# Performance work log

Measured on AMD Instinct MI355X. Metric: run time of the kernel, lower is better.

## Reference

```python
import jax, jax.numpy as jnp
import numpy as np
from jax import lax

B, T, K = 8192, 512, 5


def setup_inputs() -> dict:
    key = jax.random.key(0)
    k1, k2, k3, k4 = jax.random.split(key, 4)
    potentials = jax.random.normal(k1, (B, T, K), dtype=jnp.float32)
    transition_params = jax.random.normal(k2, (K, K), dtype=jnp.float32) * 0.1
    sequence_lengths = jax.random.randint(k3, (B,), 1, T + 1, dtype=jnp.int32)
    tag_indices = jax.random.randint(k4, (B, T), 0, K, dtype=jnp.int32)
    return {
        "potentials": potentials,
        "transition_params": transition_params,
        "sequence_lengths": sequence_lengths,
        "tag_indices": tag_indices,
    }


def _crf(potentials, transition_params, sequence_lengths, tag_indices):
    Bn, Tn, Kn = potentials.shape
    alpha0 = potentials[:, 0]                        # (B, K)
    pots_rest = jnp.swapaxes(potentials[:, 1:], 0, 1)  # (T-1, B, K)
    ts = jnp.arange(1, Tn)
    valid = ts[:, None] < sequence_lengths[None, :]    # (T-1, B)
    tag_range = jnp.arange(Kn, dtype=jnp.int32)

    # ---- Viterbi forward: max-product DP with backpointers ----
    def vit_step(alpha, inp):
        pot_t, v = inp
        scores = alpha[:, :, None] + transition_params[None]  # (B, K, K) over prev i -> next j
        bp = jnp.argmax(scores, axis=1).astype(jnp.int32)     # (B, K)
        new_alpha = jnp.max(scores, axis=1) + pot_t
        alpha = jnp.where(v[:, None], new_alpha, alpha)       # freeze past seq end
        bp = jnp.where(v[:, None], bp, tag_range[None])       # identity bp past seq end
        return alpha, bp

    alpha_v, bps = lax.scan(vit_step, alpha0, (pots_rest, valid))
    last_tag = jnp.argmax(alpha_v, axis=1).astype(jnp.int32)  # (B,)

    # ---- backtrack ----
    def back_step(tag, bp_t):
        prev = jnp.take_along_axis(bp_t, tag[:, None], axis=1)[:, 0]
        return prev, prev

    _, prev_tags = lax.scan(back_step, last_tag, bps, reverse=True)  # (T-1, B) tags 0..T-2
    decoded = jnp.concatenate([jnp.swapaxes(prev_tags, 0, 1), last_tag[:, None]], axis=1)
    mask = jnp.arange(Tn)[None] < sequence_lengths[:, None]          # (B, T)
    decoded = jnp.where(mask, decoded, 0)

    # ---- forward algorithm: log partition ----
    def fwd_step(alpha, inp):
        pot_t, v = inp
        new_alpha = jax.nn.logsumexp(alpha[:, :, None] + transition_params[None], axis=1) + pot_t
        return jnp.where(v[:, None], new_alpha, alpha), None

    alpha_f, _ = lax.scan(fwd_step, alpha0, (pots_rest, valid))
    log_norm = jax.nn.logsumexp(alpha_f, axis=1)                     # (B,)

    # ---- gold sequence score ----
    unary = jnp.take_along_axis(potentials, tag_indices[:, :, None], axis=2)[:, :, 0]  # (B, T)
    unary = jnp.sum(jnp.where(mask, unary, 0.0), axis=1)
    trans_sc = transition_params[tag_indices[:, :-1], tag_indices[:, 1:]]              # (B, T-1)
    tmask = jnp.arange(1, Tn)[None] < sequence_lengths[:, None]
    binary = jnp.sum(jnp.where(tmask, trans_sc, 0.0), axis=1)

    log_likelihood = unary + binary - log_norm
    return decoded, log_likelihood


def reference(potentials, transition_params, sequence_lengths, tag_indices):
    return _crf(potentials, transition_params, sequence_lengths, tag_indices)
```

## Files before the change

### kernel.cpp

```cpp
#include <hip/hip_runtime.h>
#include <stdint.h>

#define KK 5
#define TT 512

template<int P>
__device__ __forceinline__ float swzf(float v) {
  return __int_as_float(__builtin_amdgcn_ds_swizzle(__float_as_int(v), P));
}
template<int P>
__device__ __forceinline__ int swzi(int v) {
  return __builtin_amdgcn_ds_swizzle(v, P);
}
#define BC0 0x018
#define BC1 0x038
#define BC2 0x058
#define BC3 0x078
#define BC4 0x098
#define X1 0x041F
#define X2 0x081F
#define X4 0x101F

__device__ __forceinline__ void loadCol(float (&d)[8], const float* __restrict__ colp, int k) {
  const int t0 = k * 8 + 1;
  if (k < 63) {
#pragma unroll
    for (int s = 0; s < 8; ++s) d[s] = colp[(t0 + s) * KK];
  } else {
#pragma unroll
    for (int s = 0; s < 8; ++s) d[s] = colp[min(t0 + s, TT - 1) * KK];
  }
}

__device__ __forceinline__ void vit_map_block(const float (&pv)[8], int k, int len_eff,
                                              const float (&trc)[KK], float& a,
                                              int jj, int g, int r,
                                              uint32_t* __restrict__ s_map) {
  uint32_t bits = 0;
#pragma unroll
  for (int s = 0; s < 8; ++s) {
    const float av0 = swzf<BC0>(a), av1 = swzf<BC1>(a), av2 = swzf<BC2>(a),
                av3 = swzf<BC3>(a), av4 = swzf<BC4>(a);
    const float s0 = av0 + trc[0], s1 = av1 + trc[1], s2 = av2 + trc[2],
                s3 = av3 + trc[3], s4 = av4 + trc[4];
    const float bm = fmaxf(fmaxf(fmaxf(s0, s1), fmaxf(s2, s3)), s4);
    int bi = 4;
    bi = (s3 == bm) ? 3 : bi;
    bi = (s2 == bm) ? 2 : bi;
    bi = (s1 == bm) ? 1 : bi;
    bi = (s0 == bm) ? 0 : bi;
    const int t = k * 8 + s + 1;
    const bool act = (t < len_eff);
    a = act ? (bm + pv[s]) : a;
    const int bie = act ? bi : jj;
    bits |= (uint32_t)bie << (3 * s);
  }
  int cur = jj;
  uint32_t dec = 0;
#pragma unroll
  for (int s = 7; s >= 0; --s) {
    const int w = __builtin_amdgcn_ds_bpermute(((g << 3) + cur) << 2, (int)bits);
    const int b3 = (w >> (3 * s)) & 7;
    dec |= (uint32_t)b3 << (3 * s);
    cur = b3;
  }
  if (r < 5) s_map[g * 321 + k * 5 + jj] = dec;
}

__device__ __forceinline__ void fwd_block(const float (&pv)[8], int k, int len_eff,
                                          const float (&Wc)[KK], float& p, float& Cacc) {
#pragma unroll
  for (int s = 0; s < 8; ++s) {
    const float p0 = swzf<BC0>(p), p1 = swzf<BC1>(p), p2 = swzf<BC2>(p),
                p3 = swzf<BC3>(p), p4 = swzf<BC4>(p);
    const float u  = fmaf(p1, Wc[1], p0 * Wc[0]);
    const float v2 = fmaf(p3, Wc[3], p2 * Wc[2]);
    const float acc = fmaf(p4, Wc[4], u + v2);
    const float E = __expf(pv[s]);
    const int t = k * 8 + s + 1;
    const bool act = (t < len_eff);
    p = act ? (acc * E) : p;
  }
  float m = p;
  m = fmaxf(m, swzf<X1>(m));
  m = fmaxf(m, swzf<X2>(m));
  m = fmaxf(m, swzf<X4>(m));
  p *= (1.0f / m);
  Cacc += __logf(m);
}

__launch_bounds__(64)
__global__ void crf_kernel(const float* __restrict__ pot,
                           const float* __restrict__ trans,
                           const int* __restrict__ lens,
                           const int* __restrict__ tags,
                           float* __restrict__ out,
                           int B, int T) {
  __shared__ uint32_t s_map[8 * 321];
  __shared__ uint32_t s_chosen[8 * 65];
  const int lane = threadIdx.x;
  const int g = lane >> 3, r = lane & 7;
  const int jj = (r < 5) ? r : 4;
  const unsigned u = blockIdx.x;
  const int role = (u >> 3) & 1;
  const int idx = (int)((u & 7u) | ((u >> 4) << 3));
  const int b = idx * 8 + g;
  const int len = lens[b];
  const int len_eff = (r < 5) ? len : 0;
  const float* __restrict__ prow = pot + (size_t)b * (T * KK);
  const float* __restrict__ colp = prow + jj;

  int ml = len;
  ml = max(ml, __shfl_xor(ml, 8));
  ml = max(ml, __shfl_xor(ml, 16));
  ml = max(ml, __shfl_xor(ml, 32));
  const int nblk = (ml + 7) >> 3;

  if (role == 0) {
    float trc[KK];
#pragma unroll
    for (int i = 0; i < KK; ++i) trc[i] = trans[i * KK + jj];
    float a = (r < 5) ? prow[jj] : -3.0e38f;

    float pA[8], pB[8], pC[8];
    loadCol(pA, colp, 0);
    loadCol(pB, colp, min(1, nblk - 1));
    loadCol(pC, colp, min(2, nblk - 1));
    int blk = 0;
    while (true) {
      vit_map_block(pA, blk, len_eff, trc, a, jj, g, r, s_map);
      if (++blk == nblk) break;
      loadCol(pA, colp, min(blk + 2, nblk - 1));
      vit_map_block(pB, blk, len_eff, trc, a, jj, g, r, s_map);
      if (++blk == nblk) break;
      loadCol(pB, colp, min(blk + 2, nblk - 1));
      vit_map_block(pC, blk, len_eff, trc, a, jj, g, r, s_map);
      if (++blk == nblk) break;
      loadCol(pC, colp, min(blk + 2, nblk - 1));
    }
    float bm = a;
    bm = fmaxf(bm, swzf<X1>(bm));
    bm = fmaxf(bm, swzf<X2>(bm));
    bm = fmaxf(bm, swzf<X4>(bm));
    int cand = (r < 5 && a == bm) ? r : 7;
    cand = min(cand, swzi<X1>(cand));
    cand = min(cand, swzi<X2>(cand));
    cand = min(cand, swzi<X4>(cand));
    const int last = cand;

    __syncthreads();
    if (r == 0) {
      int tag = last;
      for (int k2 = nblk - 1; k2 >= 0; --k2) {
        const uint32_t w = s_map[g * 321 + k2 * 5 + tag];
        s_chosen[g * 65 + k2] = w;
        tag = (int)(w & 7u);
      }
    }
    __syncthreads();

    float* __restrict__ orow = out + (size_t)b * T;
#pragma unroll
    for (int kk = 0; kk < 8; ++kk) {
      const int k2 = kk * 8 + r;
      const uint32_t w = s_chosen[g * 65 + k2];
      const int base = k2 * 8;
      float f[8];
#pragma unroll
      for (int pI = 0; pI < 8; ++pI)
        f[pI] = (base + pI < len) ? (float)((w >> (3 * pI)) & 7u) : 0.0f;
      *(float4*)(orow + base)     = make_float4(f[0], f[1], f[2], f[3]);
      *(float4*)(orow + base + 4) = make_float4(f[4], f[5], f[6], f[7]);
    }

  } else {
    const float trv = trans[min(lane, 24)];
    const int* __restrict__ tgrow = tags + (size_t)b * T;
    float sc = 0.0f;
    {
      const int t0 = r * 64;
      int ptag = (t0 == 0) ? 0 : tgrow[t0 - 1];
#pragma unroll 2
      for (int q = 0; q < 16; ++q) {
        const int4 tq = *(const int4*)(tgrow + t0 + q * 4);
#pragma unroll
        for (int m = 0; m < 4; ++m) {
          const int t = t0 + q * 4 + m;
          const int ct = (m == 0) ? tq.x : (m == 1) ? tq.y : (m == 2) ? tq.z : tq.w;
          const float uadd = prow[t * KK + ct];
          const float badd = __int_as_float(__builtin_amdgcn_ds_bpermute(
              (ptag * KK + ct) << 2, __float_as_int(trv)));
          const float contrib = uadd + ((t >= 1) ? badd : 0.0f);
          sc += (t < len) ? contrib : 0.0f;
          ptag = ct;
        }
      }
    }
    sc += swzf<X1>(sc);
    sc += swzf<X2>(sc);
    sc += swzf<X4>(sc);

    float Wc[KK];
#pragma unroll
    for (int i = 0; i < KK; ++i) Wc[i] = __expf(trans[i * KK + jj]);
    float p = (r < 5) ? __expf(prow[jj]) : 0.0f;
    float Cacc = 0.0f;

    float pA[8], pB[8], pC[8];
    loadCol(pA, colp, 0);
    loadCol(pB, colp, min(1, nblk - 1));
    loadCol(pC, colp, min(2, nblk - 1));
    int blk = 0;
    while (true) {
      fwd_block(pA, blk, len_eff, Wc, p, Cacc);
      if (++blk == nblk) break;
      loadCol(pA, colp, min(blk + 2, nblk - 1));
      fwd_block(pB, blk, len_eff, Wc, p, Cacc);
      if (++blk == nblk) break;
      loadCol(pB, colp, min(blk + 2, nblk - 1));
      fwd_block(pC, blk, len_eff, Wc, p, Cacc);
      if (++blk == nblk) break;
      loadCol(pC, colp, min(blk + 2, nblk - 1));
    }
    float ps = p;
    ps += swzf<X1>(ps);
    ps += swzf<X2>(ps);
    ps += swzf<X4>(ps);
    const float logZ = Cacc + __logf(ps);
    if (r == 0) out[(size_t)B * T + b] = sc - logZ;
  }
}

extern "C" void kernel_launch(void* const* d_in, const int* in_sizes, int n_in,
                              void* d_out, int out_size, void* d_ws, size_t ws_size,
                              hipStream_t stream) {
  const float* pot   = (const float*)d_in[0];
  const float* trans = (const float*)d_in[1];
  const int*   lens  = (const int*)d_in[2];
  const int*   tags  = (const int*)d_in[3];
  float* out = (float*)d_out;

  const int B = in_sizes[2];
  const int T = in_sizes[3] / B;

  const int nblocks = 2 * (B / 8);
  crf_kernel<<<nblocks, 64, 0, stream>>>(pot, trans, lens, tags, out, B, T);
}
```

Measured before the change: 91.89 us.

## Drop per-block backpointer composition and use exponent-only rescaling in CRF kernel

The Viterbi path no longer composes 8-step backpointer maps with bpermute chains. It stores raw per-step backpointer bits and does a serial per-step backtrack in one lane per sequence, with the next block's words prefetched. Masking on the recurrence is replaced by snapshotting the state at t==len-1 (a_fin, p_fin, C_fin). The forward pass swaps its per-block cross-lane max reduction, reciprocal and log for a power-of-two rescale from ilogbf/ldexpf on the already-broadcast values, and issues its potential loads before the gold-score loop. This shortens the recurrence's dependency chain, but the backtrack becomes a longer serial loop per sequence, and removing the __syncthreads relies on s_bits and s_chosen being written and read within the same wave.

```diff
diff --git a/kernel.cpp b/kernel.cpp
--- a/kernel.cpp
+++ b/kernel.cpp
@@ -21,6 +21,16 @@
 #define X2 0x081F
 #define X4 0x101F
 
+__device__ __forceinline__ uint32_t sel5u(uint32_t w0, uint32_t w1, uint32_t w2,
+                                          uint32_t w3, uint32_t w4, int ct) {
+  uint32_t u = w0;
+  u = (ct == 1) ? w1 : u;
+  u = (ct == 2) ? w2 : u;
+  u = (ct == 3) ? w3 : u;
+  u = (ct == 4) ? w4 : u;
+  return u;
+}
+
 __device__ __forceinline__ void loadCol(float (&d)[8], const float* __restrict__ colp, int k) {
   const int t0 = k * 8 + 1;
   if (k < 63) {
@@ -32,13 +42,14 @@
   }
 }
 
-__device__ __forceinline__ void vit_map_block(const float (&pv)[8], int k, int len_eff,
-                                              const float (&trc)[KK], float& a,
-                                              int jj, int g, int r,
-                                              uint32_t* __restrict__ s_map) {
+__device__ __forceinline__ void vit_blk(const float (&pv)[8], int k, int len,
+                                        const float (&trc)[KK], float& a,
+                                        float& a_fin, int g, int r, int jj,
+                                        uint32_t* __restrict__ s_bits) {
   uint32_t bits = 0;
 #pragma unroll
   for (int s = 0; s < 8; ++s) {
+    const int t = k * 8 + s + 1;
     const float av0 = swzf<BC0>(a), av1 = swzf<BC1>(a), av2 = swzf<BC2>(a),
                 av3 = swzf<BC3>(a), av4 = swzf<BC4>(a);
     const float s0 = av0 + trc[0], s1 = av1 + trc[1], s2 = av2 + trc[2],
@@ -49,44 +60,36 @@
     bi = (s2 == bm) ? 2 : bi;
     bi = (s1 == bm) ? 1 : bi;
     bi = (s0 == bm) ? 0 : bi;
+    bits |= (uint32_t)bi << (3 * s);
+    a = bm + pv[s];
+    a_fin = (t == len - 1) ? a : a_fin;
+  }
+  if (r < 5) s_bits[g * 321 + k * 5 + jj] = bits;
+}
+
+__device__ __forceinline__ void fwd_blk(const float (&pv)[8], int k, int len,
+                                        const float (&Wc)[KK], float& p,
+                                        float& Cacc, float& p_fin, float& C_fin) {
+#pragma unroll
+  for (int s = 0; s < 8; ++s) {
     const int t = k * 8 + s + 1;
-    const bool act = (t < len_eff);
-    a = act ? (bm + pv[s]) : a;
-    const int bie = act ? bi : jj;
-    bits |= (uint32_t)bie << (3 * s);
-  }
-  int cur = jj;
-  uint32_t dec = 0;
-#pragma unroll
-  for (int s = 7; s >= 0; --s) {
-    const int w = __builtin_amdgcn_ds_bpermute(((g << 3) + cur) << 2, (int)bits);
-    const int b3 = (w >> (3 * s)) & 7;
-    dec |= (uint32_t)b3 << (3 * s);
-    cur = b3;
-  }
-  if (r < 5) s_map[g * 321 + k * 5 + jj] = dec;
-}
-
-__device__ __forceinline__ void fwd_block(const float (&pv)[8], int k, int len_eff,
-                                          const float (&Wc)[KK], float& p, float& Cacc) {
-#pragma unroll
-  for (int s = 0; s < 8; ++s) {
     const float p0 = swzf<BC0>(p), p1 = swzf<BC1>(p), p2 = swzf<BC2>(p),
                 p3 = swzf<BC3>(p), p4 = swzf<BC4>(p);
-    const float u  = fmaf(p1, Wc[1], p0 * Wc[0]);
-    const float v2 = fmaf(p3, Wc[3], p2 * Wc[2]);
-    const float acc = fmaf(p4, Wc[4], u + v2);
+    float r_ = 1.0f;
+    if (s == 0 && k > 0) {
+      const float m = fmaxf(fmaxf(fmaxf(p0, p1), fmaxf(p2, p3)), p4);
+      const int e = ilogbf(m);
+      r_ = ldexpf(1.0f, -e);
+      Cacc += (float)e * 0.69314718056f;
+    }
     const float E = __expf(pv[s]);
-    const int t = k * 8 + s + 1;
-    const bool act = (t < len_eff);
-    p = act ? (acc * E) : p;
-  }
-  float m = p;
-  m = fmaxf(m, swzf<X1>(m));
-  m = fmaxf(m, swzf<X2>(m));
-  m = fmaxf(m, swzf<X4>(m));
-  p *= (1.0f / m);
-  Cacc += __logf(m);
+    float acc = fmaf(p1, Wc[1], p0 * Wc[0]);
+    const float acc2 = fmaf(p3, Wc[3], p2 * Wc[2]);
+    acc = fmaf(p4, Wc[4], acc + acc2);
+    p = acc * E * r_;
+    p_fin = (t == len - 1) ? p : p_fin;
+    C_fin = (t == len - 1) ? Cacc : C_fin;
+  }
 }
 
 __launch_bounds__(64)
@@ -96,7 +99,7 @@
                            const int* __restrict__ tags,
                            float* __restrict__ out,
                            int B, int T) {
-  __shared__ uint32_t s_map[8 * 321];
+  __shared__ uint32_t s_bits[8 * 321];
   __shared__ uint32_t s_chosen[8 * 65];
   const int lane = threadIdx.x;
   const int g = lane >> 3, r = lane & 7;
@@ -106,7 +109,6 @@
   const int idx = (int)((u & 7u) | ((u >> 4) << 3));
   const int b = idx * 8 + g;
   const int len = lens[b];
-  const int len_eff = (r < 5) ? len : 0;
   const float* __restrict__ prow = pot + (size_t)b * (T * KK);
   const float* __restrict__ colp = prow + jj;
 
@@ -121,6 +123,7 @@
 #pragma unroll
     for (int i = 0; i < KK; ++i) trc[i] = trans[i * KK + jj];
     float a = (r < 5) ? prow[jj] : -3.0e38f;
+    float a_fin = a;
 
     float pA[8], pB[8], pC[8];
     loadCol(pA, colp, 0);
@@ -128,36 +131,59 @@
     loadCol(pC, colp, min(2, nblk - 1));
     int blk = 0;
     while (true) {
-      vit_map_block(pA, blk, len_eff, trc, a, jj, g, r, s_map);
+      vit_blk(pA, blk, len, trc, a, a_fin, g, r, jj, s_bits);
       if (++blk == nblk) break;
       loadCol(pA, colp, min(blk + 2, nblk - 1));
-      vit_map_block(pB, blk, len_eff, trc, a, jj, g, r, s_map);
+      vit_blk(pB, blk, len, trc, a, a_fin, g, r, jj, s_bits);
       if (++blk == nblk) break;
       loadCol(pB, colp, min(blk + 2, nblk - 1));
-      vit_map_block(pC, blk, len_eff, trc, a, jj, g, r, s_map);
+      vit_blk(pC, blk, len, trc, a, a_fin, g, r, jj, s_bits);
       if (++blk == nblk) break;
       loadCol(pC, colp, min(blk + 2, nblk - 1));
     }
-    float bm = a;
+    float bm = a_fin;
     bm = fmaxf(bm, swzf<X1>(bm));
     bm = fmaxf(bm, swzf<X2>(bm));
     bm = fmaxf(bm, swzf<X4>(bm));
-    int cand = (r < 5 && a == bm) ? r : 7;
+    int cand = (r < 5 && a_fin == bm) ? r : 7;
     cand = min(cand, swzi<X1>(cand));
     cand = min(cand, swzi<X2>(cand));
     cand = min(cand, swzi<X4>(cand));
     const int last = cand;
 
-    __syncthreads();
     if (r == 0) {
       int tag = last;
-      for (int k2 = nblk - 1; k2 >= 0; --k2) {
-        const uint32_t w = s_map[g * 321 + k2 * 5 + tag];
-        s_chosen[g * 65 + k2] = w;
-        tag = (int)(w & 7u);
+      uint32_t acc = (uint32_t)last << (3 * ((len - 1) & 7));
+      int kcur = (len - 1) >> 3;
+      const uint32_t* __restrict__ bb = s_bits + g * 321;
+      int kb = (len - 2) >> 3;
+      uint32_t w0 = 0, w1 = 0, w2 = 0, w3 = 0, w4 = 0;
+      if (kb >= 0) {
+        w0 = bb[kb * 5 + 0]; w1 = bb[kb * 5 + 1]; w2 = bb[kb * 5 + 2];
+        w3 = bb[kb * 5 + 3]; w4 = bb[kb * 5 + 4];
       }
-    }
-    __syncthreads();
+      for (; kb >= 0; --kb) {
+        uint32_t n0 = 0, n1 = 0, n2 = 0, n3 = 0, n4 = 0;
+        if (kb > 0) {
+          n0 = bb[(kb - 1) * 5 + 0]; n1 = bb[(kb - 1) * 5 + 1];
+          n2 = bb[(kb - 1) * 5 + 2]; n3 = bb[(kb - 1) * 5 + 3];
+          n4 = bb[(kb - 1) * 5 + 4];
+        }
+#pragma unroll
+        for (int s = 7; s >= 0; --s) {
+          const int t = kb * 8 + s + 1;
+          if (t <= len - 1) {
+            const uint32_t w = sel5u(w0, w1, w2, w3, w4, tag);
+            const int prev = (int)((w >> (3 * s)) & 7u);
+            if (kb != kcur) { s_chosen[g * 65 + kcur] = acc; acc = 0; kcur = kb; }
+            acc |= (uint32_t)prev << (3 * s);
+            tag = prev;
+          }
+        }
+        w0 = n0; w1 = n1; w2 = n2; w3 = n3; w4 = n4;
+      }
+      s_chosen[g * 65 + kcur] = acc;
+    }
 
     float* __restrict__ orow = out + (size_t)b * T;
 #pragma unroll
@@ -174,6 +200,11 @@
     }
 
   } else {
+    float pA[8], pB[8], pC[8];
+    loadCol(pA, colp, 0);
+    loadCol(pB, colp, min(1, nblk - 1));
+    loadCol(pC, colp, min(2, nblk - 1));
+
     const float trv = trans[min(lane, 24)];
     const int* __restrict__ tgrow = tags + (size_t)b * T;
     float sc = 0.0f;
@@ -205,28 +236,25 @@
     for (int i = 0; i < KK; ++i) Wc[i] = __expf(trans[i * KK + jj]);
     float p = (r < 5) ? __expf(prow[jj]) : 0.0f;
     float Cacc = 0.0f;
-
-    float pA[8], pB[8], pC[8];
-    loadCol(pA, colp, 0);
-    loadCol(pB, colp, min(1, nblk - 1));
-    loadCol(pC, colp, min(2, nblk - 1));
+    float p_fin = p, C_fin = 0.0f;
+
     int blk = 0;
     while (true) {
-      fwd_block(pA, blk, len_eff, Wc, p, Cacc);
+      fwd_blk(pA, blk, len, Wc, p, Cacc, p_fin, C_fin);
       if (++blk == nblk) break;
       loadCol(pA, colp, min(blk + 2, nblk - 1));
-      fwd_block(pB, blk, len_eff, Wc, p, Cacc);
+      fwd_blk(pB, blk, len, Wc, p, Cacc, p_fin, C_fin);
       if (++blk == nblk) break;
       loadCol(pB, colp, min(blk + 2, nblk - 1));
-      fwd_block(pC, blk, len_eff, Wc, p, Cacc);
+      fwd_blk(pC, blk, len, Wc, p, Cacc, p_fin, C_fin);
       if (++blk == nblk) break;
       loadCol(pC, colp, min(blk + 2, nblk - 1));
     }
-    float ps = p;
+    float ps = (r < 5) ? p_fin : 0.0f;
     ps += swzf<X1>(ps);
     ps += swzf<X2>(ps);
     ps += swzf<X4>(ps);
-    const float logZ = Cacc + __logf(ps);
+    const float logZ = C_fin + __logf(ps);
     if (r == 0) out[(size_t)B * T + b] = sc - logZ;
   }
 }
```

After: 115.0 us. 1.25x slower.

## Merge Viterbi and forward roles into one two-wave block, fuse gold score

Applied to the files above, without the earlier changes.

The two separate 64-thread blocks per group of 8 sequences become one 128-thread block. Wave 0 runs Viterbi and wave 1 runs the forward algorithm, and they share results through LDS with block barriers. The gold-sequence score is now computed inside the Viterbi loop from the potentials already held in registers plus prefetched tags. This removes the second wave's separate strided re-read of potentials and its bpermute-based transition lookups. The backtrack also gains special handling for the block containing the last valid step, which adds serial work on one lane and a dependency between the two waves.

```diff
diff --git a/kernel.cpp b/kernel.cpp
--- a/kernel.cpp
+++ b/kernel.cpp
@@ -4,12 +4,10 @@
 #define KK 5
 #define TT 512
 
-template<int P>
-__device__ __forceinline__ float swzf(float v) {
+template<int P> __device__ __forceinline__ float swzf(float v) {
   return __int_as_float(__builtin_amdgcn_ds_swizzle(__float_as_int(v), P));
 }
-template<int P>
-__device__ __forceinline__ int swzi(int v) {
+template<int P> __device__ __forceinline__ int swzi(int v) {
   return __builtin_amdgcn_ds_swizzle(v, P);
 }
 #define BC0 0x018
@@ -21,9 +19,21 @@
 #define X2 0x081F
 #define X4 0x101F
 
+__device__ __forceinline__ float sel5f(float v0,float v1,float v2,float v3,float v4,int ct){
+  float u=v0; u=(ct==1)?v1:u; u=(ct==2)?v2:u; u=(ct==3)?v3:u; u=(ct==4)?v4:u; return u;
+}
+__device__ __forceinline__ uint32_t sel5u(uint32_t w0,uint32_t w1,uint32_t w2,uint32_t w3,uint32_t w4,int ct){
+  uint32_t u=w0; u=(ct==1)?w1:u; u=(ct==2)?w2:u; u=(ct==3)?w3:u; u=(ct==4)?w4:u; return u;
+}
+__device__ __forceinline__ int telt(const int4 (&tp)[2], int s) {
+  const int4 v = (s < 4) ? tp[0] : tp[1];
+  const int m = s & 3;
+  return m == 0 ? v.x : (m == 1 ? v.y : (m == 2 ? v.z : v.w));
+}
+
 __device__ __forceinline__ void loadCol(float (&d)[8], const float* __restrict__ colp, int k) {
   const int t0 = k * 8 + 1;
-  if (k < 63) {
+  if (k < TT / 8 - 1) {
 #pragma unroll
     for (int s = 0; s < 8; ++s) d[s] = colp[(t0 + s) * KK];
   } else {
@@ -31,11 +41,15 @@
     for (int s = 0; s < 8; ++s) d[s] = colp[min(t0 + s, TT - 1) * KK];
   }
 }
-
-__device__ __forceinline__ void vit_map_block(const float (&pv)[8], int k, int len_eff,
-                                              const float (&trc)[KK], float& a,
-                                              int jj, int g, int r,
-                                              uint32_t* __restrict__ s_map) {
+__device__ __forceinline__ void loadTag(int4 (&tp)[2], const int* __restrict__ tg, int k) {
+  tp[0] = *(const int4*)(tg + 8 * k);
+  tp[1] = *(const int4*)(tg + 8 * k + 4);
+}
+
+__device__ __forceinline__ void vit_map_block(const float (&pv)[8], const int4 (&tp)[2],
+    int k, int len, int len_eff, const float (&trc)[KK], float& a,
+    float& pvcar, int& tagcar, float& usum, float& bsum,
+    int jj, int g, int r, uint32_t* __restrict__ s_map) {
   uint32_t bits = 0;
 #pragma unroll
   for (int s = 0; s < 8; ++s) {
@@ -65,10 +79,22 @@
     cur = b3;
   }
   if (r < 5) s_map[g * 321 + k * 5 + jj] = dec;
-}
-
-__device__ __forceinline__ void fwd_block(const float (&pv)[8], int k, int len_eff,
-                                          const float (&Wc)[KK], float& p, float& Cacc) {
+#pragma unroll
+  for (int s2 = 0; s2 < 8; ++s2) {
+    const int t = k * 8 + s2;
+    const int ct = telt(tp, s2);
+    const int pt = (s2 == 0) ? tagcar : telt(tp, s2 - 1);
+    const float potv = (s2 == 0) ? pvcar : pv[s2 - 1];
+    const bool um = (t < len) && (ct == r);
+    usum += um ? potv : 0.0f;
+    bsum += (um && t >= 1) ? sel5f(trc[0], trc[1], trc[2], trc[3], trc[4], pt) : 0.0f;
+  }
+  pvcar = pv[7];
+  tagcar = telt(tp, 7);
+}
+
+__device__ __forceinline__ void fwd_blk(const float (&pv)[8], int k, int len_eff,
+                                        const float (&Wc)[KK], float& p, float& Cacc) {
 #pragma unroll
   for (int s = 0; s < 8; ++s) {
     const float p0 = swzf<BC0>(p), p1 = swzf<BC1>(p), p2 = swzf<BC2>(p),
@@ -89,7 +115,7 @@
   Cacc += __logf(m);
 }
 
-__launch_bounds__(64)
+__launch_bounds__(128)
 __global__ void crf_kernel(const float* __restrict__ pot,
                            const float* __restrict__ trans,
                            const int* __restrict__ lens,
@@ -98,13 +124,13 @@
                            int B, int T) {
   __shared__ uint32_t s_map[8 * 321];
   __shared__ uint32_t s_chosen[8 * 65];
-  const int lane = threadIdx.x;
+  __shared__ float s_sc[8];
+  const int tid = threadIdx.x;
+  const int wave = tid >> 6;
+  const int lane = tid & 63;
   const int g = lane >> 3, r = lane & 7;
   const int jj = (r < 5) ? r : 4;
-  const unsigned u = blockIdx.x;
-  const int role = (u >> 3) & 1;
-  const int idx = (int)((u & 7u) | ((u >> 4) << 3));
-  const int b = idx * 8 + g;
+  const int b = blockIdx.x * 8 + g;
   const int len = lens[b];
   const int len_eff = (r < 5) ? len : 0;
   const float* __restrict__ prow = pot + (size_t)b * (T * KK);
@@ -116,28 +142,41 @@
   ml = max(ml, __shfl_xor(ml, 32));
   const int nblk = (ml + 7) >> 3;
 
-  if (role == 0) {
+  int last = 0;
+  float logZ = 0.0f;
+
+  if (wave == 0) {
     float trc[KK];
 #pragma unroll
     for (int i = 0; i < KK; ++i) trc[i] = trans[i * KK + jj];
     float a = (r < 5) ? prow[jj] : -3.0e38f;
+    float usum = 0.0f, bsum = 0.0f;
+    float pvcar = prow[jj];
+    int tagcar = 0;
+    const int* __restrict__ tg = tags + (size_t)b * T;
 
     float pA[8], pB[8], pC[8];
-    loadCol(pA, colp, 0);
-    loadCol(pB, colp, min(1, nblk - 1));
-    loadCol(pC, colp, min(2, nblk - 1));
+    int4 TA[2], TB[2], TC[2];
+    loadCol(pA, colp, 0);               loadTag(TA, tg, 0);
+    loadCol(pB, colp, min(1, nblk - 1)); loadTag(TB, tg, min(1, nblk - 1));
+    loadCol(pC, colp, min(2, nblk - 1)); loadTag(TC, tg, min(2, nblk - 1));
     int blk = 0;
     while (true) {
-      vit_map_block(pA, blk, len_eff, trc, a, jj, g, r, s_map);
-      if (++blk == nblk) break;
-      loadCol(pA, colp, min(blk + 2, nblk - 1));
-      vit_map_block(pB, blk, len_eff, trc, a, jj, g, r, s_map);
-      if (++blk == nblk) break;
-      loadCol(pB, colp, min(blk + 2, nblk - 1));
-      vit_map_block(pC, blk, len_eff, trc, a, jj, g, r, s_map);
-      if (++blk == nblk) break;
-      loadCol(pC, colp, min(blk + 2, nblk - 1));
-    }
+      vit_map_block(pA, TA, blk, len, len_eff, trc, a, pvcar, tagcar, usum, bsum, jj, g, r, s_map);
+      if (++blk == nblk) break;
+      loadCol(pA, colp, min(blk + 2, nblk - 1)); loadTag(TA, tg, min(blk + 2, nblk - 1));
+      vit_map_block(pB, TB, blk, len, len_eff, trc, a, pvcar, tagcar, usum, bsum, jj, g, r, s_map);
+      if (++blk == nblk) break;
+      loadCol(pB, colp, min(blk + 2, nblk - 1)); loadTag(TB, tg, min(blk + 2, nblk - 1));
+      vit_map_block(pC, TC, blk, len, len_eff, trc, a, pvcar, tagcar, usum, bsum, jj, g, r, s_map);
+      if (++blk == nblk) break;
+      loadCol(pC, colp, min(blk + 2, nblk - 1)); loadTag(TC, tg, min(blk + 2, nblk - 1));
+    }
+    float sc = usum + bsum;
+    sc += swzf<X1>(sc);
+    sc += swzf<X2>(sc);
+    sc += swzf<X4>(sc);
+    if (r == 0) s_sc[g] = sc;
     float bm = a;
     bm = fmaxf(bm, swzf<X1>(bm));
     bm = fmaxf(bm, swzf<X2>(bm));
@@ -146,79 +185,26 @@
     cand = min(cand, swzi<X1>(cand));
     cand = min(cand, swzi<X2>(cand));
     cand = min(cand, swzi<X4>(cand));
-    const int last = cand;
-
-    __syncthreads();
-    if (r == 0) {
-      int tag = last;
-      for (int k2 = nblk - 1; k2 >= 0; --k2) {
-        const uint32_t w = s_map[g * 321 + k2 * 5 + tag];
-        s_chosen[g * 65 + k2] = w;
-        tag = (int)(w & 7u);
-      }
-    }
-    __syncthreads();
-
-    float* __restrict__ orow = out + (size_t)b * T;
-#pragma unroll
-    for (int kk = 0; kk < 8; ++kk) {
-      const int k2 = kk * 8 + r;
-      const uint32_t w = s_chosen[g * 65 + k2];
-      const int base = k2 * 8;
-      float f[8];
-#pragma unroll
-      for (int pI = 0; pI < 8; ++pI)
-        f[pI] = (base + pI < len) ? (float)((w >> (3 * pI)) & 7u) : 0.0f;
-      *(float4*)(orow + base)     = make_float4(f[0], f[1], f[2], f[3]);
-      *(float4*)(orow + base + 4) = make_float4(f[4], f[5], f[6], f[7]);
-    }
-
+    last = cand;
   } else {
-    const float trv = trans[min(lane, 24)];
-    const int* __restrict__ tgrow = tags + (size_t)b * T;
-    float sc = 0.0f;
-    {
-      const int t0 = r * 64;
-      int ptag = (t0 == 0) ? 0 : tgrow[t0 - 1];
-#pragma unroll 2
-      for (int q = 0; q < 16; ++q) {
-        const int4 tq = *(const int4*)(tgrow + t0 + q * 4);
-#pragma unroll
-        for (int m = 0; m < 4; ++m) {
-          const int t = t0 + q * 4 + m;
-          const int ct = (m == 0) ? tq.x : (m == 1) ? tq.y : (m == 2) ? tq.z : tq.w;
-          const float uadd = prow[t * KK + ct];
-          const float badd = __int_as_float(__builtin_amdgcn_ds_bpermute(
-              (ptag * KK + ct) << 2, __float_as_int(trv)));
-          const float contrib = uadd + ((t >= 1) ? badd : 0.0f);
-          sc += (t < len) ? contrib : 0.0f;
-          ptag = ct;
-        }
-      }
-    }
-    sc += swzf<X1>(sc);
-    sc += swzf<X2>(sc);
-    sc += swzf<X4>(sc);
-
     float Wc[KK];
 #pragma unroll
     for (int i = 0; i < KK; ++i) Wc[i] = __expf(trans[i * KK + jj]);
     float p = (r < 5) ? __expf(prow[jj]) : 0.0f;
     float Cacc = 0.0f;
-
     float pA[8], pB[8], pC[8];
     loadCol(pA, colp, 0);
     loadCol(pB, colp, min(1, nblk - 1));
     loadCol(pC, colp, min(2, nblk - 1));
     int blk = 0;
     while (true) {
-      fwd_block(pA, blk, len_eff, Wc, p, Cacc);
+      fwd_blk(pA, blk, len_eff, Wc, p, Cacc);
       if (++blk == nblk) break;
       loadCol(pA, colp, min(blk + 2, nblk - 1));
-      fwd_block(pB, blk, len_eff, Wc, p, Cacc);
+      fwd_blk(pB, blk, len_eff, Wc, p, Cacc);
       if (++blk == nblk) break;
       loadCol(pB, colp, min(blk + 2, nblk - 1));
-      fwd_block(pC, blk, len_eff, Wc, p, Cacc);
+      fwd_blk(pC, blk, len_eff, Wc, p, Cacc);
       if (++blk == nblk) break;
       loadCol(pC, colp, min(blk + 2, nblk - 1));
     }
@@ -226,8 +212,59 @@
     ps += swzf<X1>(ps);
     ps += swzf<X2>(ps);
     ps += swzf<X4>(ps);
-    const float logZ = Cacc + __logf(ps);
-    if (r == 0) out[(size_t)B * T + b] = sc - logZ;
+    logZ = Cacc + __logf(ps);
+  }
+
+  __syncthreads();
+
+  if (wave == 0) {
+    if (r == 0) {
+      int tag = last;
+      uint32_t acc = (uint32_t)last << (3 * ((len - 1) & 7));
+      int kcur = (len - 1) >> 3;
+      const uint32_t* __restrict__ bb = s_map + g * 321;
+      for (int k2 = nblk - 1; k2 >= 0; --k2) {
+        if (k2 < kcur) {
+          const uint32_t w = bb[k2 * 5 + tag];
+          s_chosen[g * 65 + k2] = w;
+          tag = (int)(w & 7u);
+        } else if (k2 == kcur) {
+          const uint32_t w = bb[k2 * 5 + tag];
+          uint32_t best = acc;
+          const int sl = (len - 1) & 7;
+#pragma unroll
+          for (int cnd = 0; cnd < 5; ++cnd) {
+            const uint32_t wr = bb[k2 * 5 + cnd];
+            if (((int)((wr >> (3 * sl)) & 7u)) == tag) {
+              const uint32_t mask = (sl > 0) ? ((1u << (3 * sl)) - 1u) : 0u;
+              best = (wr & mask) | ((uint32_t)tag << (3 * sl));
+            }
+          }
+          s_chosen[g * 65 + k2] = best;
+          tag = (int)(best & 7u);
+        }
+      }
+    }
+  } else {
+    if (r == 0) out[(size_t)B * T + b] = s_sc[g] - logZ;
+  }
+
+  __syncthreads();
+
+  if (wave == 0) {
+    float* __restrict__ orow = out + (size_t)b * T;
+#pragma unroll
+    for (int kk = 0; kk < 8; ++kk) {
+      const int k2 = kk * 8 + r;
+      const uint32_t w = s_chosen[g * 65 + k2];
+      const int base = k2 * 8;
+      float f[8];
+#pragma unroll
+      for (int pI = 0; pI < 8; ++pI)
+        f[pI] = (base + pI < len) ? (float)((w >> (3 * pI)) & 7u) : 0.0f;
+      *(float4*)(orow + base)     = make_float4(f[0], f[1], f[2], f[3]);
+      *(float4*)(orow + base + 4) = make_float4(f[4], f[5], f[6], f[7]);
+    }
   }
 }
 
@@ -243,6 +280,5 @@
   const int B = in_sizes[2];
   const int T = in_sizes[3] / B;
 
-  const int nblocks = 2 * (B / 8);
-  crf_kernel<<<nblocks, 64, 0, stream>>>(pot, trans, lens, tags, out, B, T);
-}
+  crf_kernel<<<B / 8, 128, 0, stream>>>(pot, trans, lens, tags, out, B, T);
+}
```

Result: slower. 121.3 us (+32.0%).

## Fuse gold-score into forward pass and parallelize Viterbi in-block backtrack

Applied to the files above, without the earlier changes.

The gold-sequence score is now accumulated inside the forward-algorithm block loop. It reuses the potentials already loaded per column and prefetched tag vectors, replacing the separate gather loop with its per-step bpermute of transition values. In the Viterbi map step, the serial chain of eight dependent ds_bpermute calls becomes five independent bpermutes followed by register selects, shortening the dependency latency. The two __syncthreads around the backtrack are dropped, relying on the 64-thread block being a single wavefront; this is a correctness risk if LDS ordering is not guaranteed.

```diff
diff --git a/kernel.cpp b/kernel.cpp
--- a/kernel.cpp
+++ b/kernel.cpp
@@ -4,12 +4,10 @@
 #define KK 5
 #define TT 512
 
-template<int P>
-__device__ __forceinline__ float swzf(float v) {
+template<int P> __device__ __forceinline__ float swzf(float v) {
   return __int_as_float(__builtin_amdgcn_ds_swizzle(__float_as_int(v), P));
 }
-template<int P>
-__device__ __forceinline__ int swzi(int v) {
+template<int P> __device__ __forceinline__ int swzi(int v) {
   return __builtin_amdgcn_ds_swizzle(v, P);
 }
 #define BC0 0x018
@@ -21,15 +19,31 @@
 #define X2 0x081F
 #define X4 0x101F
 
+__device__ __forceinline__ float sel5f(float v0,float v1,float v2,float v3,float v4,int ct){
+  float u=v0; u=(ct==1)?v1:u; u=(ct==2)?v2:u; u=(ct==3)?v3:u; u=(ct==4)?v4:u; return u;
+}
+__device__ __forceinline__ uint32_t sel5u(uint32_t w0,uint32_t w1,uint32_t w2,uint32_t w3,uint32_t w4,int ct){
+  uint32_t u=w0; u=(ct==1)?w1:u; u=(ct==2)?w2:u; u=(ct==3)?w3:u; u=(ct==4)?w4:u; return u;
+}
+__device__ __forceinline__ int telt(const int4 (&tp)[2], int s) {
+  const int4 v = (s < 4) ? tp[0] : tp[1];
+  const int m = s & 3;
+  return m == 0 ? v.x : (m == 1 ? v.y : (m == 2 ? v.z : v.w));
+}
+
 __device__ __forceinline__ void loadCol(float (&d)[8], const float* __restrict__ colp, int k) {
   const int t0 = k * 8 + 1;
-  if (k < 63) {
+  if (k < TT / 8 - 1) {
 #pragma unroll
     for (int s = 0; s < 8; ++s) d[s] = colp[(t0 + s) * KK];
   } else {
 #pragma unroll
     for (int s = 0; s < 8; ++s) d[s] = colp[min(t0 + s, TT - 1) * KK];
   }
+}
+__device__ __forceinline__ void loadTag(int4 (&tp)[2], const int* __restrict__ tg, int k) {
+  tp[0] = *(const int4*)(tg + 8 * k);
+  tp[1] = *(const int4*)(tg + 8 * k + 4);
 }
 
 __device__ __forceinline__ void vit_map_block(const float (&pv)[8], int k, int len_eff,
@@ -55,20 +69,29 @@
     const int bie = act ? bi : jj;
     bits |= (uint32_t)bie << (3 * s);
   }
+  const uint32_t w0 = (uint32_t)__builtin_amdgcn_ds_bpermute(((g << 3) + 0) << 2, (int)bits);
+  const uint32_t w1 = (uint32_t)__builtin_amdgcn_ds_bpermute(((g << 3) + 1) << 2, (int)bits);
+  const uint32_t w2 = (uint32_t)__builtin_amdgcn_ds_bpermute(((g << 3) + 2) << 2, (int)bits);
+  const uint32_t w3 = (uint32_t)__builtin_amdgcn_ds_bpermute(((g << 3) + 3) << 2, (int)bits);
+  const uint32_t w4 = (uint32_t)__builtin_amdgcn_ds_bpermute(((g << 3) + 4) << 2, (int)bits);
   int cur = jj;
   uint32_t dec = 0;
 #pragma unroll
   for (int s = 7; s >= 0; --s) {
-    const int w = __builtin_amdgcn_ds_bpermute(((g << 3) + cur) << 2, (int)bits);
-    const int b3 = (w >> (3 * s)) & 7;
+    const uint32_t w = sel5u(w0, w1, w2, w3, w4, cur);
+    const int b3 = (int)((w >> (3 * s)) & 7u);
     dec |= (uint32_t)b3 << (3 * s);
     cur = b3;
   }
   if (r < 5) s_map[g * 321 + k * 5 + jj] = dec;
 }
 
-__device__ __forceinline__ void fwd_block(const float (&pv)[8], int k, int len_eff,
-                                          const float (&Wc)[KK], float& p, float& Cacc) {
+__device__ __forceinline__ void fwd_blk(const float (&pv)[8], const int4 (&tp)[2],
+                                        int k, int len, int len_eff,
+                                        const float (&Wc)[KK], const float (&trcR)[KK],
+                                        float& p, float& Cacc,
+                                        float& pvcar, int& tagcar,
+                                        float& usum, float& bsum, int r) {
 #pragma unroll
   for (int s = 0; s < 8; ++s) {
     const float p0 = swzf<BC0>(p), p1 = swzf<BC1>(p), p2 = swzf<BC2>(p),
@@ -81,6 +104,18 @@
     const bool act = (t < len_eff);
     p = act ? (acc * E) : p;
   }
+#pragma unroll
+  for (int s2 = 0; s2 < 8; ++s2) {
+    const int t = k * 8 + s2;
+    const int ct = telt(tp, s2);
+    const int pt = (s2 == 0) ? tagcar : telt(tp, s2 - 1);
+    const float potv = (s2 == 0) ? pvcar : pv[s2 - 1];
+    const bool um = (t < len) && (ct == r);
+    usum += um ? potv : 0.0f;
+    bsum += (um && t >= 1) ? sel5f(trcR[0], trcR[1], trcR[2], trcR[3], trcR[4], pt) : 0.0f;
+  }
+  pvcar = pv[7];
+  tagcar = telt(tp, 7);
   float m = p;
   m = fmaxf(m, swzf<X1>(m));
   m = fmaxf(m, swzf<X2>(m));
@@ -148,7 +183,6 @@
     cand = min(cand, swzi<X4>(cand));
     const int last = cand;
 
-    __syncthreads();
     if (r == 0) {
       int tag = last;
       for (int k2 = nblk - 1; k2 >= 0; --k2) {
@@ -157,7 +191,6 @@
         tag = (int)(w & 7u);
       }
     }
-    __syncthreads();
 
     float* __restrict__ orow = out + (size_t)b * T;
 #pragma unroll
@@ -174,54 +207,41 @@
     }
 
   } else {
-    const float trv = trans[min(lane, 24)];
-    const int* __restrict__ tgrow = tags + (size_t)b * T;
-    float sc = 0.0f;
-    {
-      const int t0 = r * 64;
-      int ptag = (t0 == 0) ? 0 : tgrow[t0 - 1];
-#pragma unroll 2
-      for (int q = 0; q < 16; ++q) {
-        const int4 tq = *(const int4*)(tgrow + t0 + q * 4);
-#pragma unroll
-        for (int m = 0; m < 4; ++m) {
-          const int t = t0 + q * 4 + m;
-          const int ct = (m == 0) ? tq.x : (m == 1) ? tq.y : (m == 2) ? tq.z : tq.w;
-          const float uadd = prow[t * KK + ct];
-          const float badd = __int_as_float(__builtin_amdgcn_ds_bpermute(
-              (ptag * KK + ct) << 2, __float_as_int(trv)));
-          const float contrib = uadd + ((t >= 1) ? badd : 0.0f);
-          sc += (t < len) ? contrib : 0.0f;
-          ptag = ct;
-        }
-      }
-    }
+    float Wc[KK], trcR[KK];
+#pragma unroll
+    for (int i = 0; i < KK; ++i) {
+      trcR[i] = trans[i * KK + jj];
+      Wc[i] = __expf(trcR[i]);
+    }
+    const float pj0 = prow[jj];
+    float p = (r < 5) ? __expf(pj0) : 0.0f;
+    float Cacc = 0.0f;
+    float usum = 0.0f, bsum = 0.0f;
+    float pvcar = pj0;
+    int tagcar = 0;
+    const int* __restrict__ tg = tags + (size_t)b * T;
+
+    float pA[8], pB[8], pC[8];
+    int4 TA[2], TB[2], TC[2];
+    loadCol(pA, colp, 0);                loadTag(TA, tg, 0);
+    loadCol(pB, colp, min(1, nblk - 1)); loadTag(TB, tg, min(1, nblk - 1));
+    loadCol(pC, colp, min(2, nblk - 1)); loadTag(TC, tg, min(2, nblk - 1));
+    int blk = 0;
+    while (true) {
+      fwd_blk(pA, TA, blk, len, len_eff, Wc, trcR, p, Cacc, pvcar, tagcar, usum, bsum, r);
+      if (++blk == nblk) break;
+      loadCol(pA, colp, min(blk + 2, nblk - 1)); loadTag(TA, tg, min(blk + 2, nblk - 1));
+      fwd_blk(pB, TB, blk, len, len_eff, Wc, trcR, p, Cacc, pvcar, tagcar, usum, bsum, r);
+      if (++blk == nblk) break;
+      loadCol(pB, colp, min(blk + 2, nblk - 1)); loadTag(TB, tg, min(blk + 2, nblk - 1));
+      fwd_blk(pC, TC, blk, len, len_eff, Wc, trcR, p, Cacc, pvcar, tagcar, usum, bsum, r);
+      if (++blk == nblk) break;
+      loadCol(pC, colp, min(blk + 2, nblk - 1)); loadTag(TC, tg, min(blk + 2, nblk - 1));
+    }
+    float sc = usum + bsum;
     sc += swzf<X1>(sc);
     sc += swzf<X2>(sc);
     sc += swzf<X4>(sc);
-
-    float Wc[KK];
-#pragma unroll
-    for (int i = 0; i < KK; ++i) Wc[i] = __expf(trans[i * KK + jj]);
-    float p = (r < 5) ? __expf(prow[jj]) : 0.0f;
-    float Cacc = 0.0f;
-
-    float pA[8], pB[8], pC[8];
-    loadCol(pA, colp, 0);
-    loadCol(pB, colp, min(1, nblk - 1));
-    loadCol(pC, colp, min(2, nblk - 1));
-    int blk = 0;
-    while (true) {
-      fwd_block(pA, blk, len_eff, Wc, p, Cacc);
-      if (++blk == nblk) break;
-      loadCol(pA, colp, min(blk + 2, nblk - 1));
-      fwd_block(pB, blk, len_eff, Wc, p, Cacc);
-      if (++blk == nblk) break;
-      loadCol(pB, colp, min(blk + 2, nblk - 1));
-      fwd_block(pC, blk, len_eff, Wc, p, Cacc);
-      if (++blk == nblk) break;
-      loadCol(pC, colp, min(blk + 2, nblk - 1));
-    }
     float ps = p;
     ps += swzf<X1>(ps);
     ps += swzf<X2>(ps);
```

Result: faster. 88.98 us (-3.2%).
